# Performance work log

Hardware: AMD Instinct MI355X
Metric: run time of the kernel (lower is better)

## Reference

```python
import jax, jax.numpy as jnp
import numpy as np

ENC_DIM = 1024
NUM_HEADS = 16
HEAD_DIM = ENC_DIM // NUM_HEADS
D_FF = 4 * ENC_DIM
EPS = 1e-5


def _layernorm(x, g, b):
    mu = jnp.mean(x, axis=-1, keepdims=True)
    var = jnp.mean((x - mu) ** 2, axis=-1, keepdims=True)
    return (x - mu) * jax.lax.rsqrt(var + EPS) * g + b


def setup_inputs() -> dict:
    key = jax.random.key(0)
    ks = jax.random.split(key, 12)
    s = 1.0 / np.sqrt(ENC_DIM)
    sf = 1.0 / np.sqrt(D_FF)
    x = jax.random.normal(ks[0], (2, 2048, ENC_DIM), dtype=jnp.float32)
    return {
        "x": x,
        "ln1_g": jnp.ones((ENC_DIM,), jnp.float32),
        "ln1_b": jnp.zeros((ENC_DIM,), jnp.float32),
        "wq": jax.random.uniform(ks[1], (ENC_DIM, ENC_DIM), jnp.float32, -s, s),
        "bq": jax.random.uniform(ks[2], (ENC_DIM,), jnp.float32, -s, s),
        "wk": jax.random.uniform(ks[3], (ENC_DIM, ENC_DIM), jnp.float32, -s, s),
        "bk": jax.random.uniform(ks[4], (ENC_DIM,), jnp.float32, -s, s),
        "wv": jax.random.uniform(ks[5], (ENC_DIM, ENC_DIM), jnp.float32, -s, s),
        "bv": jax.random.uniform(ks[6], (ENC_DIM,), jnp.float32, -s, s),
        "wo": jax.random.uniform(ks[7], (ENC_DIM, ENC_DIM), jnp.float32, -s, s),
        "bo": jax.random.uniform(ks[8], (ENC_DIM,), jnp.float32, -s, s),
        "w1": jax.random.uniform(ks[9], (ENC_DIM, D_FF), jnp.float32, -s, s),
        "b1": jax.random.uniform(ks[10], (D_FF,), jnp.float32, -s, s),
        "w2": jax.random.uniform(ks[11], (D_FF, ENC_DIM), jnp.float32, -sf, sf),
        "b2": jnp.zeros((ENC_DIM,), jnp.float32),
        "ln2_g": jnp.ones((ENC_DIM,), jnp.float32),
        "ln2_b": jnp.zeros((ENC_DIM,), jnp.float32),
    }


def reference(x, ln1_g, ln1_b, wq, bq, wk, bk, wv, bv, wo, bo, w1, b1, w2, b2, ln2_g, ln2_b):
    B, S, D = x.shape
    h = _layernorm(x, ln1_g, ln1_b)
    # QKV projections -> (B, H, S, hd)
    def split_heads(t):
        return t.reshape(B, S, NUM_HEADS, HEAD_DIM).transpose(0, 2, 1, 3)
    q = split_heads(h @ wq + bq)
    k = split_heads(h @ wk + bk)
    v = split_heads(h @ wv + bv)
    scores = jnp.einsum("bhqd,bhkd->bhqk", q, k) / np.sqrt(HEAD_DIM)
    probs = jax.nn.softmax(scores, axis=-1)
    attn = jnp.einsum("bhqk,bhkd->bhqd", probs, v)
    attn = attn.transpose(0, 2, 1, 3).reshape(B, S, D)
    x = attn @ wo + bo + x  # residual 1
    h2 = _layernorm(x, ln2_g, ln2_b)
    mlp = jax.nn.gelu(h2 @ w1 + b1, approximate=False) @ w2 + b2
    return x + mlp
```

## Files before the change

kernel.cpp:

```cpp
#include <hip/hip_runtime.h>

typedef unsigned short u16;
typedef unsigned int u32;
typedef __bf16 bf16x8 __attribute__((ext_vector_type(8)));
typedef float floatx4 __attribute__((ext_vector_type(4)));

__device__ __forceinline__ u16 f2bf(float f) {
    u32 u = __float_as_uint(f);
    u = (u + 0x7FFFu + ((u >> 16) & 1u)) >> 16;
    return (u16)u;
}

__device__ __forceinline__ void gld_lds16(const u16* g, u16* l) {
    __builtin_amdgcn_global_load_lds(
        (const __attribute__((address_space(1))) u32*)g,
        (__attribute__((address_space(3))) u32*)l, 16, 0, 0);
}

__device__ __forceinline__ float gelu_exact(float v) {
    const float z = fabsf(v) * 0.70710678118f;
    const float t = __builtin_amdgcn_rcpf(1.0f + 0.3275911f * z);
    const float e = __builtin_amdgcn_exp2f(-z * z * 1.44269504f);
    float poly = 1.061405429f;
    poly = poly * t - 1.453152027f;
    poly = poly * t + 1.421413741f;
    poly = poly * t - 0.284496736f;
    poly = poly * t + 0.254829592f;
    float erfz = 1.0f - poly * t * e;
    erfz = copysignf(erfz, v);
    return 0.5f * v * (1.0f + erfz);
}

__global__ __launch_bounds__(256) void transpose_cvt4(
    const float* __restrict__ s0, const float* __restrict__ s1,
    const float* __restrict__ s2, const float* __restrict__ s3,
    u16* __restrict__ d0, u16* __restrict__ d1,
    u16* __restrict__ d2, u16* __restrict__ d3)
{
    __shared__ float t[32][33];
    const int z = blockIdx.z;
    const float* src = z == 0 ? s0 : (z == 1 ? s1 : (z == 2 ? s2 : s3));
    u16* dst = z == 0 ? d0 : (z == 1 ? d1 : (z == 2 ? d2 : d3));
    const int bm = blockIdx.x * 32, bk = blockIdx.y * 32;
    const int tx = threadIdx.x & 31, ty = threadIdx.x >> 5;
    #pragma unroll
    for (int i = ty; i < 32; i += 8)
        t[i][tx] = src[(long)(bk + i) * 1024 + bm + tx];
    __syncthreads();
    #pragma unroll
    for (int i = ty; i < 32; i += 8)
        dst[(long)(bm + i) * 1024 + bk + tx] = f2bf(t[tx][i]);
}

__global__ __launch_bounds__(256) void transpose_cvt(
    const float* __restrict__ src, u16* __restrict__ dst, int K, int M)
{
    __shared__ float t[32][33];
    const int bm = blockIdx.x * 32, bk = blockIdx.y * 32;
    const int tx = threadIdx.x & 31, ty = threadIdx.x >> 5;
    #pragma unroll
    for (int i = ty; i < 32; i += 8)
        t[i][tx] = src[(long)(bk + i) * M + bm + tx];
    __syncthreads();
    #pragma unroll
    for (int i = ty; i < 32; i += 8)
        dst[(long)(bm + i) * K + bk + tx] = f2bf(t[tx][i]);
}

__global__ __launch_bounds__(256) void ln_kernel(
    const float* __restrict__ x, const float* __restrict__ g,
    const float* __restrict__ bta, u16* __restrict__ out)
{
    const int row = blockIdx.x;
    const int tid = threadIdx.x;
    const float4 v = ((const float4*)(x + (long)row * 1024))[tid];
    float s  = v.x + v.y + v.z + v.w;
    float s2 = v.x*v.x + v.y*v.y + v.z*v.z + v.w*v.w;
    #pragma unroll
    for (int off = 1; off < 64; off <<= 1) {
        s  += __shfl_xor(s, off);
        s2 += __shfl_xor(s2, off);
    }
    __shared__ float red[8];
    const int wave = tid >> 6, lane = tid & 63;
    if (lane == 0) { red[wave] = s; red[4 + wave] = s2; }
    __syncthreads();
    s  = red[0] + red[1] + red[2] + red[3];
    s2 = red[4] + red[5] + red[6] + red[7];
    const float mu   = s * (1.0f / 1024.0f);
    const float var  = s2 * (1.0f / 1024.0f) - mu * mu;
    const float rstd = rsqrtf(var + 1e-5f);
    const int c = tid << 2;
    ushort4 o;
    o.x = f2bf((v.x - mu) * rstd * g[c + 0] + bta[c + 0]);
    o.y = f2bf((v.y - mu) * rstd * g[c + 1] + bta[c + 1]);
    o.z = f2bf((v.z - mu) * rstd * g[c + 2] + bta[c + 2]);
    o.w = f2bf((v.w - mu) * rstd * g[c + 3] + bta[c + 3]);
    ((ushort4*)(out + (long)row * 1024))[tid] = o;
}

__global__ __launch_bounds__(256) void add_kernel(
    float* __restrict__ out, const float* __restrict__ p1)
{
    const int t = blockIdx.x * 256 + threadIdx.x;
    const float4 a = ((const float4*)out)[t];
    const float4 c = ((const float4*)p1)[t];
    float4 o;
    o.x = a.x + c.x;
    o.y = a.y + c.y;
    o.z = a.z + c.z;
    o.w = a.w + c.w;
    ((float4*)out)[t] = o;
}

__global__ __launch_bounds__(256) void vtrans_kernel(
    const u16* __restrict__ V, u16* __restrict__ Vt)
{
    __shared__ u16 t[64][72];
    const int bh = blockIdx.y, s0 = blockIdx.x << 6;
    const int tid = threadIdx.x;
    const long base = (long)bh * 2048 * 64;
    const int row = tid >> 2, seg = tid & 3;
    *(uint4*)&t[row][seg << 3] =
        *(const uint4*)(V + base + (long)(s0 + row) * 64 + (seg << 3));
    *(uint4*)&t[row][(seg + 4) << 3] =
        *(const uint4*)(V + base + (long)(s0 + row) * 64 + ((seg + 4) << 3));
    __syncthreads();
    #pragma unroll
    for (int half = 0; half < 2; ++half) {
        const int sl = (seg + (half << 2)) << 3;
        u16 tmp[8];
        #pragma unroll
        for (int j = 0; j < 8; ++j) tmp[j] = t[sl + j][row];
        *(uint4*)(Vt + base + (long)row * 2048 + s0 + sl) = *(uint4*)tmp;
    }
}

template<int MODE, int BN>
__global__ __launch_bounds__(256) void gemm_kernel(
    const u16* __restrict__ A, const u16* __restrict__ Bt,
    const float* __restrict__ bias0, const float* __restrict__ bias1,
    const float* __restrict__ bias2, const float* __restrict__ res,
    float* __restrict__ part1, void* __restrict__ outv, int K, int M)
{
    constexpr int MS  = (BN == 128) ? 4 : 2;
    constexpr int NIB = (BN == 128) ? 4 : 2;
    constexpr int DB  = (BN == 128) ? 2 : 1;
    __shared__ u16 As[DB][128 * 64];
    __shared__ u16 Bs[DB][BN * 64];
    const int tid = threadIdx.x, lane = tid & 63, wave = tid >> 6;
    const int wm = (BN == 128) ? ((wave >> 1) << 6) : (wave << 5);
    const int wn = (BN == 128) ? ((wave & 1) << 6) : 0;
    const int lrow = lane & 15, quad = lane >> 4;
    const int sl = lrow & 7;

    const int nwg = gridDim.x * gridDim.y * gridDim.z;
    const int lin = blockIdx.x + gridDim.x * (blockIdx.y + gridDim.y * blockIdx.z);
    const int wg  = (lin & 7) * (nwg >> 3) + (lin >> 3);
    const int bx  = wg % gridDim.x;
    const int rest = wg / gridDim.x;
    const int by  = rest % gridDim.y;
    const int bz  = rest / gridDim.y;

    const long rowbase = (long)by * 128;
    const long colbase = (long)bx * BN;
    int kstart = 0, kend = K;
    if constexpr (MODE == 3) {
        kstart = bz * (K >> 1);
        kend   = kstart + (K >> 1);
    }

    const u16* gA[4]; int lA[4];
    #pragma unroll
    for (int i = 0; i < 4; ++i) {
        const int cid = (i << 6) + lane;
        const int rl = cid >> 3, p = cid & 7, q = p ^ (rl & 7);
        gA[i] = A + (rowbase + (wave << 5) + rl) * (long)K + kstart + (q << 3);
        lA[i] = ((wave << 5) + rl) * 64 + (p << 3);
    }
    const u16* gB[NIB]; int lB[NIB];
    #pragma unroll
    for (int i = 0; i < NIB; ++i) {
        const int cid = (i << 6) + lane;
        const int rl = cid >> 3, p = cid & 7, q = p ^ (rl & 7);
        const int rw = (BN == 128) ? (wave << 5) : (wave << 4);
        gB[i] = Bt + (colbase + rw + rl) * (long)K + kstart + (q << 3);
        lB[i] = (rw + rl) * 64 + (p << 3);
    }

    floatx4 acc[MS][4];
    #pragma unroll
    for (int i = 0; i < MS; ++i)
        #pragma unroll
        for (int j = 0; j < 4; ++j)
            acc[i][j] = floatx4{0.f, 0.f, 0.f, 0.f};

    if constexpr (DB == 2) {
        #pragma unroll
        for (int i = 0; i < 4; ++i) { gld_lds16(gA[i], As[0] + lA[i]); gA[i] += 64; }
        #pragma unroll
        for (int i = 0; i < NIB; ++i) { gld_lds16(gB[i], Bs[0] + lB[i]); gB[i] += 64; }

        const int niter = (kend - kstart) >> 6;
        int cur = 0;
        for (int t = 0; t < niter; ++t) {
            if (t + 1 < niter) {
                #pragma unroll
                for (int i = 0; i < 4; ++i) { gld_lds16(gA[i], As[cur ^ 1] + lA[i]); gA[i] += 64; }
                #pragma unroll
                for (int i = 0; i < NIB; ++i) { gld_lds16(gB[i], Bs[cur ^ 1] + lB[i]); gB[i] += 64; }
                asm volatile("s_waitcnt vmcnt(8)" ::: "memory");
            } else {
                asm volatile("s_waitcnt vmcnt(0)" ::: "memory");
            }
            __builtin_amdgcn_s_barrier();

            const u16* as = As[cur];
            const u16* bs = Bs[cur];
            #pragma unroll
            for (int kc = 0; kc < 2; ++kc) {
                const int ph = (((kc << 2) + quad) ^ sl) << 3;
                bf16x8 af[MS], bf[4];
                #pragma unroll
                for (int ms = 0; ms < MS; ++ms)
                    af[ms] = *(const bf16x8*)&as[(wm + (ms << 4) + lrow) * 64 + ph];
                #pragma unroll
                for (int ns = 0; ns < 4; ++ns)
                    bf[ns] = *(const bf16x8*)&bs[(wn + (ns << 4) + lrow) * 64 + ph];
                #pragma unroll
                for (int ms = 0; ms < MS; ++ms)
                    #pragma unroll
                    for (int ns = 0; ns < 4; ++ns)
                        acc[ms][ns] = __builtin_amdgcn_mfma_f32_16x16x32_bf16(
                            af[ms], bf[ns], acc[ms][ns], 0, 0, 0);
            }
            asm volatile("s_waitcnt lgkmcnt(0)" ::: "memory");
            __builtin_amdgcn_s_barrier();
            cur ^= 1;
        }
    } else {
        for (int k0 = kstart; k0 < kend; k0 += 64) {
            __syncthreads();
            #pragma unroll
            for (int i = 0; i < 4; ++i) { gld_lds16(gA[i], As[0] + lA[i]); gA[i] += 64; }
            #pragma unroll
            for (int i = 0; i < NIB; ++i) { gld_lds16(gB[i], Bs[0] + lB[i]); gB[i] += 64; }
            __syncthreads();
            #pragma unroll
            for (int kc = 0; kc < 2; ++kc) {
                const int ph = (((kc << 2) + quad) ^ sl) << 3;
                bf16x8 af[MS], bf[4];
                #pragma unroll
                for (int ms = 0; ms < MS; ++ms)
                    af[ms] = *(const bf16x8*)&As[0][(wm + (ms << 4) + lrow) * 64 + ph];
                #pragma unroll
                for (int ns = 0; ns < 4; ++ns)
                    bf[ns] = *(const bf16x8*)&Bs[0][(wn + (ns << 4) + lrow) * 64 + ph];
                #pragma unroll
                for (int ms = 0; ms < MS; ++ms)
                    #pragma unroll
                    for (int ns = 0; ns < 4; ++ns)
                        acc[ms][ns] = __builtin_amdgcn_mfma_f32_16x16x32_bf16(
                            af[ms], bf[ns], acc[ms][ns], 0, 0, 0);
            }
        }
    }

    float* tgt = nullptr;
    if constexpr (MODE == 3) tgt = bz ? part1 : (float*)outv;
    #pragma unroll
    for (int ms = 0; ms < MS; ++ms) {
        #pragma unroll
        for (int ns = 0; ns < 4; ++ns) {
            const long col = colbase + wn + (ns << 4) + lrow;
            float bv = 0.f;
            if constexpr (MODE == 0) {
                const int which = (int)(col >> 10);
                const float* bp = which == 0 ? bias0 : (which == 1 ? bias1 : bias2);
                bv = bp[col & 1023];
            } else if constexpr (MODE == 1 || MODE == 2) {
                bv = bias0[col];
            }
            #pragma unroll
            for (int r = 0; r < 4; ++r) {
                const long row = rowbase + wm + (ms << 4) + (quad << 2) + r;
                float v = acc[ms][ns][r] + bv;
                if constexpr (MODE == 0) {
                    const long which = col >> 10;
                    if (which == 0) v *= 0.18033688f;
                    const long b = row >> 11, s = row & 2047;
                    const long h = (col >> 6) & 15, d = col & 63;
                    ((u16*)outv)[which * 4194304 + (((b << 4) + h) * 2048 + s) * 64 + d] = f2bf(v);
                } else if constexpr (MODE == 1) {
                    const long idx = row * M + col;
                    ((float*)outv)[idx] = v + res[idx];
                } else if constexpr (MODE == 2) {
                    ((u16*)outv)[row * M + col] = f2bf(gelu_exact(v));
                } else {
                    const long idx = row * M + col;
                    if (bz == 0)
                        tgt[idx] = v + bias0[col] + res[idx];
                    else
                        tgt[idx] = v;
                }
            }
        }
    }
}

__global__ __launch_bounds__(512) void attn_kernel(
    const u16* __restrict__ Q, const u16* __restrict__ Kp,
    const u16* __restrict__ Vt, u16* __restrict__ O)
{
    __shared__ u16 Ks[2][4096];
    __shared__ u16 Vs[2][4096];
    __shared__ u16 Ps[8][16][72];
    const int tid = threadIdx.x, lane = tid & 63, wave = tid >> 6;
    const int lrow = lane & 15, quad = lane >> 4;

    const int lin = blockIdx.x;
    const int nl  = ((lin & 7) << 6) + (lin >> 3);
    const int bh  = nl >> 4;
    const int qt  = nl & 15;
    const long kvbase = (long)bh * 2048 * 64;
    const int qbase = (qt << 7) + (wave << 4);

    const int srow = lane >> 3;
    const int schunk = (lane & 7) ^ srow;
    const int c = wave & 3;
    const bool isV = wave >= 4;
    const int lofs = c << 10;
    const u16* g0 = isV
        ? (Vt + kvbase + (long)(((c << 4) + srow) * 2048 + (schunk << 3)))
        : (Kp + kvbase + (long)(((c << 4) + srow) * 64   + (schunk << 3)));
    const u16* g1 = g0 + (isV ? 8 * 2048 : 8 * 64);
    const int gstep = isV ? 64 : 4096;
    u16* lb0 = isV ? &Vs[0][lofs] : &Ks[0][lofs];
    u16* lb1 = isV ? &Vs[1][lofs] : &Ks[1][lofs];

    bf16x8 qf[2];
    #pragma unroll
    for (int h = 0; h < 2; ++h)
        qf[h] = *(const bf16x8*)(Q + kvbase +
            (long)(qbase + lrow) * 64 + (quad << 3) + (h << 5));

    int aoff[4][2];
    #pragma unroll
    for (int ns = 0; ns < 4; ++ns)
        #pragma unroll
        for (int h = 0; h < 2; ++h)
            aoff[ns][h] = ((ns << 4) + lrow) * 64 +
                          (((quad + (h << 2)) ^ (lrow & 7)) << 3);

    floatx4 oacc[4];
    #pragma unroll
    for (int ns = 0; ns < 4; ++ns)
        oacc[ns] = floatx4{0.f, 0.f, 0.f, 0.f};
    float lr = 0.f;

    gld_lds16(g0, lb0);
    gld_lds16(g1, lb0 + 512);
    g0 += gstep; g1 += gstep;

    for (int it = 0; it < 32; ++it) {
        const int cur = it & 1;
        __syncthreads();
        if (it < 31) {
            u16* dst = cur ? lb0 : lb1;
            gld_lds16(g0, dst);
            gld_lds16(g1, dst + 512);
            g0 += gstep; g1 += gstep;
        }
        const u16* ks = &Ks[cur][0];
        const u16* vs = &Vs[cur][0];

        floatx4 st[4];
        __builtin_amdgcn_s_setprio(1);
        #pragma unroll
        for (int ns = 0; ns < 4; ++ns) {
            const bf16x8 af0 = *(const bf16x8*)&ks[aoff[ns][0]];
            const bf16x8 af1 = *(const bf16x8*)&ks[aoff[ns][1]];
            floatx4 z = floatx4{0.f, 0.f, 0.f, 0.f};
            st[ns] = __builtin_amdgcn_mfma_f32_16x16x32_bf16(af0, qf[0], z, 0, 0, 0);
            st[ns] = __builtin_amdgcn_mfma_f32_16x16x32_bf16(af1, qf[1], st[ns], 0, 0, 0);
        }
        __builtin_amdgcn_s_setprio(0);

        float rs = 0.f;
        #pragma unroll
        for (int ns = 0; ns < 4; ++ns) {
            const float p0 = __builtin_amdgcn_exp2f(st[ns][0]);
            const float p1 = __builtin_amdgcn_exp2f(st[ns][1]);
            const float p2 = __builtin_amdgcn_exp2f(st[ns][2]);
            const float p3 = __builtin_amdgcn_exp2f(st[ns][3]);
            rs += (p0 + p1) + (p2 + p3);
            uint2 w;
            w.x = __builtin_amdgcn_perm(__float_as_uint(p1) + 0x8000u,
                                        __float_as_uint(p0) + 0x8000u, 0x07060302u);
            w.y = __builtin_amdgcn_perm(__float_as_uint(p3) + 0x8000u,
                                        __float_as_uint(p2) + 0x8000u, 0x07060302u);
            *(uint2*)&Ps[wave][lrow][(ns << 4) + (quad << 2)] = w;
        }
        rs += __shfl_xor(rs, 16);
        rs += __shfl_xor(rs, 32);
        lr += rs;
        const bf16x8 pf0 = *(const bf16x8*)&Ps[wave][lrow][quad << 3];
        const bf16x8 pf1 = *(const bf16x8*)&Ps[wave][lrow][(quad << 3) + 32];

        __builtin_amdgcn_s_setprio(1);
        #pragma unroll
        for (int ns = 0; ns < 4; ++ns) {
            const bf16x8 vf0 = *(const bf16x8*)&vs[aoff[ns][0]];
            const bf16x8 vf1 = *(const bf16x8*)&vs[aoff[ns][1]];
            oacc[ns] = __builtin_amdgcn_mfma_f32_16x16x32_bf16(pf0, vf0, oacc[ns], 0, 0, 0);
            oacc[ns] = __builtin_amdgcn_mfma_f32_16x16x32_bf16(pf1, vf1, oacc[ns], 0, 0, 0);
        }
        __builtin_amdgcn_s_setprio(0);
    }

    const int b = bh >> 4, h = bh & 15;
    float linv[4];
    #pragma unroll
    for (int r = 0; r < 4; ++r)
        linv[r] = 1.0f / __shfl(lr, (quad << 2) + r);
    #pragma unroll
    for (int ns = 0; ns < 4; ++ns)
        #pragma unroll
        for (int r = 0; r < 4; ++r) {
            const int q = qbase + (quad << 2) + r;
            const long token = (long)b * 2048 + q;
            O[token * 1024 + (h << 6) + (ns << 4) + lrow] =
                f2bf(oacc[ns][r] * linv[r]);
        }
}

extern "C" void kernel_launch(void* const* d_in, const int* in_sizes, int n_in,
                              void* d_out, int out_size, void* d_ws, size_t ws_size,
                              hipStream_t stream)
{
    const float* x     = (const float*)d_in[0];
    const float* ln1_g = (const float*)d_in[1];
    const float* ln1_b = (const float*)d_in[2];
    const float* wq    = (const float*)d_in[3];
    const float* bq    = (const float*)d_in[4];
    const float* wk    = (const float*)d_in[5];
    const float* bk    = (const float*)d_in[6];
    const float* wv    = (const float*)d_in[7];
    const float* bv    = (const float*)d_in[8];
    const float* wo    = (const float*)d_in[9];
    const float* bo    = (const float*)d_in[10];
    const float* w1    = (const float*)d_in[11];
    const float* b1    = (const float*)d_in[12];
    const float* w2    = (const float*)d_in[13];
    const float* b2    = (const float*)d_in[14];
    const float* ln2_g = (const float*)d_in[15];
    const float* ln2_b = (const float*)d_in[16];
    float* out = (float*)d_out;

    char* w = (char*)d_ws;
    const size_t MB = 1024 * 1024;
    u16*   wqkvt = (u16*)(w + 0);
    u16*   wot   = (u16*)(w + 6  * MB);
    u16*   w1t   = (u16*)(w + 8  * MB);
    u16*   w2t   = (u16*)(w + 16 * MB);
    u16*   h1    = (u16*)(w + 24 * MB);
    u16*   qkvb  = (u16*)(w + 32 * MB);
    u16*   vtb   = (u16*)(w + 56 * MB);
    float* x1    = (float*)(w + 64 * MB);
    float* part1 = (float*)(w + 80 * MB);
    u16*   ffb   = (u16*)(w + 32 * MB);
    u16*   qb = qkvb;
    u16*   kb = qkvb + 4194304;
    u16*   vb = qkvb + 8388608;

    transpose_cvt4<<<dim3(32, 32, 4), 256, 0, stream>>>(
        wq, wk, wv, wo, wqkvt, wqkvt + 1048576, wqkvt + 2097152, wot);
    transpose_cvt<<<dim3(128, 32), 256, 0, stream>>>(w1, w1t, 1024, 4096);
    transpose_cvt<<<dim3(32, 128), 256, 0, stream>>>(w2, w2t, 4096, 1024);

    ln_kernel<<<4096, 256, 0, stream>>>(x, ln1_g, ln1_b, h1);

    gemm_kernel<0, 128><<<dim3(24, 32), 256, 0, stream>>>(
        h1, wqkvt, bq, bk, bv, nullptr, nullptr, qkvb, 1024, 3072);

    vtrans_kernel<<<dim3(32, 32), 256, 0, stream>>>(vb, vtb);

    attn_kernel<<<dim3(512), 512, 0, stream>>>(qb, kb, vtb, h1);

    gemm_kernel<1, 64><<<dim3(16, 32), 256, 0, stream>>>(
        h1, wot, bo, nullptr, nullptr, x, nullptr, x1, 1024, 1024);

    ln_kernel<<<4096, 256, 0, stream>>>(x1, ln2_g, ln2_b, h1);

    gemm_kernel<2, 128><<<dim3(32, 32), 256, 0, stream>>>(
        h1, w1t, b1, nullptr, nullptr, nullptr, nullptr, ffb, 1024, 4096);

    gemm_kernel<3, 128><<<dim3(8, 32, 2), 256, 0, stream>>>(
        ffb, w2t, b2, nullptr, nullptr, x1, part1, out, 4096, 1024);

    add_kernel<<<4096, 256, 0, stream>>>(out, part1);
}
```

Baseline: 372.9 us.

## Use 256x256 tiled GEMM with 8 waves and atomic split-K for FFN down

Replaces the 128-row GEMM kernel with a 512-thread 256x256 tile kernel (double-buffered LDS, setprio around MFMA bursts) for QKV, FFN-up and FFN-down, which raises data reuse per tile. FFN-down now uses 4-way split-K accumulated via float atomicAdd into a memset output, replacing the separate partial buffer and add kernel. The O-projection keeps the old 64-wide tile path as a standalone kernel. Larger tiles reduce the number of workgroups and may hurt occupancy, and float atomics make the summation order nondeterministic.

```diff
diff --git a/kernel.cpp b/kernel.cpp
--- a/kernel.cpp
+++ b/kernel.cpp
@@ -99,20 +99,6 @@
     ((ushort4*)(out + (long)row * 1024))[tid] = o;
 }
 
-__global__ __launch_bounds__(256) void add_kernel(
-    float* __restrict__ out, const float* __restrict__ p1)
-{
-    const int t = blockIdx.x * 256 + threadIdx.x;
-    const float4 a = ((const float4*)out)[t];
-    const float4 c = ((const float4*)p1)[t];
-    float4 o;
-    o.x = a.x + c.x;
-    o.y = a.y + c.y;
-    o.z = a.z + c.z;
-    o.w = a.w + c.w;
-    ((float4*)out)[t] = o;
-}
-
 __global__ __launch_bounds__(256) void vtrans_kernel(
     const u16* __restrict__ V, u16* __restrict__ Vt)
 {
@@ -136,23 +122,18 @@
     }
 }
 
-template<int MODE, int BN>
-__global__ __launch_bounds__(256) void gemm_kernel(
+template<int MODE>
+__global__ __launch_bounds__(512, 2) void gemm256_kernel(
     const u16* __restrict__ A, const u16* __restrict__ Bt,
     const float* __restrict__ bias0, const float* __restrict__ bias1,
     const float* __restrict__ bias2, const float* __restrict__ res,
-    float* __restrict__ part1, void* __restrict__ outv, int K, int M)
-{
-    constexpr int MS  = (BN == 128) ? 4 : 2;
-    constexpr int NIB = (BN == 128) ? 4 : 2;
-    constexpr int DB  = (BN == 128) ? 2 : 1;
-    __shared__ u16 As[DB][128 * 64];
-    __shared__ u16 Bs[DB][BN * 64];
+    float* __restrict__ outf, void* __restrict__ outv, int K, int M)
+{
+    __shared__ u16 As[2][256 * 64];
+    __shared__ u16 Bs[2][256 * 64];
     const int tid = threadIdx.x, lane = tid & 63, wave = tid >> 6;
-    const int wm = (BN == 128) ? ((wave >> 1) << 6) : (wave << 5);
-    const int wn = (BN == 128) ? ((wave & 1) << 6) : 0;
-    const int lrow = lane & 15, quad = lane >> 4;
-    const int sl = lrow & 7;
+    const int wr = wave >> 2, wc = wave & 3;
+    const int lrow = lane & 15, quad = lane >> 4, sl = lrow & 7;
 
     const int nwg = gridDim.x * gridDim.y * gridDim.z;
     const int lin = blockIdx.x + gridDim.x * (blockIdx.y + gridDim.y * blockIdx.z);
@@ -162,128 +143,103 @@
     const int by  = rest % gridDim.y;
     const int bz  = rest / gridDim.y;
 
-    const long rowbase = (long)by * 128;
-    const long colbase = (long)bx * BN;
+    const long rowbase = (long)by * 256;
+    const long colbase = (long)bx * 256;
     int kstart = 0, kend = K;
-    if constexpr (MODE == 3) {
-        kstart = bz * (K >> 1);
-        kend   = kstart + (K >> 1);
-    }
+    if constexpr (MODE == 3) { kstart = bz * (K >> 2); kend = kstart + (K >> 2); }
 
     const u16* gA[4]; int lA[4];
+    const u16* gB[4]; int lB[4];
     #pragma unroll
     for (int i = 0; i < 4; ++i) {
-        const int cid = (i << 6) + lane;
+        const int cid = (i << 9) + tid;
         const int rl = cid >> 3, p = cid & 7, q = p ^ (rl & 7);
-        gA[i] = A + (rowbase + (wave << 5) + rl) * (long)K + kstart + (q << 3);
-        lA[i] = ((wave << 5) + rl) * 64 + (p << 3);
-    }
-    const u16* gB[NIB]; int lB[NIB];
-    #pragma unroll
-    for (int i = 0; i < NIB; ++i) {
-        const int cid = (i << 6) + lane;
-        const int rl = cid >> 3, p = cid & 7, q = p ^ (rl & 7);
-        const int rw = (BN == 128) ? (wave << 5) : (wave << 4);
-        gB[i] = Bt + (colbase + rw + rl) * (long)K + kstart + (q << 3);
-        lB[i] = (rw + rl) * 64 + (p << 3);
-    }
-
-    floatx4 acc[MS][4];
-    #pragma unroll
-    for (int i = 0; i < MS; ++i)
+        gA[i] = A  + (rowbase + rl) * (long)K + kstart + (q << 3);
+        gB[i] = Bt + (colbase + rl) * (long)K + kstart + (q << 3);
+        lA[i] = rl * 64 + (p << 3);
+        lB[i] = rl * 64 + (p << 3);
+    }
+
+    floatx4 acc[8][4];
+    #pragma unroll
+    for (int i = 0; i < 8; ++i)
         #pragma unroll
         for (int j = 0; j < 4; ++j)
             acc[i][j] = floatx4{0.f, 0.f, 0.f, 0.f};
 
-    if constexpr (DB == 2) {
-        #pragma unroll
-        for (int i = 0; i < 4; ++i) { gld_lds16(gA[i], As[0] + lA[i]); gA[i] += 64; }
-        #pragma unroll
-        for (int i = 0; i < NIB; ++i) { gld_lds16(gB[i], Bs[0] + lB[i]); gB[i] += 64; }
-
-        const int niter = (kend - kstart) >> 6;
-        int cur = 0;
-        for (int t = 0; t < niter; ++t) {
-            if (t + 1 < niter) {
+    #pragma unroll
+    for (int i = 0; i < 4; ++i) { gld_lds16(gA[i], As[0] + lA[i]); gA[i] += 64; }
+    #pragma unroll
+    for (int i = 0; i < 4; ++i) { gld_lds16(gB[i], Bs[0] + lB[i]); gB[i] += 64; }
+    asm volatile("s_waitcnt vmcnt(0)" ::: "memory");
+    __builtin_amdgcn_s_barrier();
+    __builtin_amdgcn_sched_barrier(0);
+
+    const int niter = (kend - kstart) >> 6;
+    int cur = 0;
+    for (int t = 0; t < niter; ++t) {
+        if (t + 1 < niter) {
+            #pragma unroll
+            for (int i = 0; i < 4; ++i) { gld_lds16(gA[i], As[cur ^ 1] + lA[i]); gA[i] += 64; }
+            #pragma unroll
+            for (int i = 0; i < 4; ++i) { gld_lds16(gB[i], Bs[cur ^ 1] + lB[i]); gB[i] += 64; }
+        }
+
+        const u16* as = As[cur];
+        const u16* bs = Bs[cur];
+
+        bf16x8 bfr[4][2];
+        #pragma unroll
+        for (int ns = 0; ns < 4; ++ns)
+            #pragma unroll
+            for (int kc = 0; kc < 2; ++kc)
+                bfr[ns][kc] = *(const bf16x8*)
+                    &bs[((wc << 6) + (ns << 4) + lrow) * 64 + ((((kc << 2) + quad) ^ sl) << 3)];
+
+        #pragma unroll
+        for (int p = 0; p < 4; ++p) {
+            bf16x8 af[2][2];
+            #pragma unroll
+            for (int m = 0; m < 2; ++m)
                 #pragma unroll
-                for (int i = 0; i < 4; ++i) { gld_lds16(gA[i], As[cur ^ 1] + lA[i]); gA[i] += 64; }
+                for (int kc = 0; kc < 2; ++kc)
+                    af[m][kc] = *(const bf16x8*)
+                        &as[((wr << 7) + ((p * 2 + m) << 4) + lrow) * 64 + ((((kc << 2) + quad) ^ sl) << 3)];
+            __builtin_amdgcn_s_setprio(1);
+            #pragma unroll
+            for (int kc = 0; kc < 2; ++kc)
                 #pragma unroll
-                for (int i = 0; i < NIB; ++i) { gld_lds16(gB[i], Bs[cur ^ 1] + lB[i]); gB[i] += 64; }
-                asm volatile("s_waitcnt vmcnt(8)" ::: "memory");
-            } else {
-                asm volatile("s_waitcnt vmcnt(0)" ::: "memory");
-            }
-            __builtin_amdgcn_s_barrier();
-
-            const u16* as = As[cur];
-            const u16* bs = Bs[cur];
-            #pragma unroll
-            for (int kc = 0; kc < 2; ++kc) {
-                const int ph = (((kc << 2) + quad) ^ sl) << 3;
-                bf16x8 af[MS], bf[4];
-                #pragma unroll
-                for (int ms = 0; ms < MS; ++ms)
-                    af[ms] = *(const bf16x8*)&as[(wm + (ms << 4) + lrow) * 64 + ph];
-                #pragma unroll
-                for (int ns = 0; ns < 4; ++ns)
-                    bf[ns] = *(const bf16x8*)&bs[(wn + (ns << 4) + lrow) * 64 + ph];
-                #pragma unroll
-                for (int ms = 0; ms < MS; ++ms)
+                for (int m = 0; m < 2; ++m)
                     #pragma unroll
                     for (int ns = 0; ns < 4; ++ns)
-                        acc[ms][ns] = __builtin_amdgcn_mfma_f32_16x16x32_bf16(
-                            af[ms], bf[ns], acc[ms][ns], 0, 0, 0);
-            }
-            asm volatile("s_waitcnt lgkmcnt(0)" ::: "memory");
-            __builtin_amdgcn_s_barrier();
-            cur ^= 1;
-        }
-    } else {
-        for (int k0 = kstart; k0 < kend; k0 += 64) {
-            __syncthreads();
-            #pragma unroll
-            for (int i = 0; i < 4; ++i) { gld_lds16(gA[i], As[0] + lA[i]); gA[i] += 64; }
-            #pragma unroll
-            for (int i = 0; i < NIB; ++i) { gld_lds16(gB[i], Bs[0] + lB[i]); gB[i] += 64; }
-            __syncthreads();
-            #pragma unroll
-            for (int kc = 0; kc < 2; ++kc) {
-                const int ph = (((kc << 2) + quad) ^ sl) << 3;
-                bf16x8 af[MS], bf[4];
-                #pragma unroll
-                for (int ms = 0; ms < MS; ++ms)
-                    af[ms] = *(const bf16x8*)&As[0][(wm + (ms << 4) + lrow) * 64 + ph];
-                #pragma unroll
-                for (int ns = 0; ns < 4; ++ns)
-                    bf[ns] = *(const bf16x8*)&Bs[0][(wn + (ns << 4) + lrow) * 64 + ph];
-                #pragma unroll
-                for (int ms = 0; ms < MS; ++ms)
-                    #pragma unroll
-                    for (int ns = 0; ns < 4; ++ns)
-                        acc[ms][ns] = __builtin_amdgcn_mfma_f32_16x16x32_bf16(
-                            af[ms], bf[ns], acc[ms][ns], 0, 0, 0);
-            }
-        }
-    }
-
-    float* tgt = nullptr;
-    if constexpr (MODE == 3) tgt = bz ? part1 : (float*)outv;
-    #pragma unroll
-    for (int ms = 0; ms < MS; ++ms) {
+                        acc[p * 2 + m][ns] = __builtin_amdgcn_mfma_f32_16x16x32_bf16(
+                            af[m][kc], bfr[ns][kc], acc[p * 2 + m][ns], 0, 0, 0);
+            __builtin_amdgcn_s_setprio(0);
+        }
+
+        asm volatile("s_waitcnt lgkmcnt(0)" ::: "memory");
+        asm volatile("s_waitcnt vmcnt(0)" ::: "memory");
+        __builtin_amdgcn_s_barrier();
+        __builtin_amdgcn_sched_barrier(0);
+        cur ^= 1;
+    }
+
+    #pragma unroll
+    for (int ms = 0; ms < 8; ++ms) {
         #pragma unroll
         for (int ns = 0; ns < 4; ++ns) {
-            const long col = colbase + wn + (ns << 4) + lrow;
+            const long col = colbase + (wc << 6) + (ns << 4) + lrow;
             float bv = 0.f;
             if constexpr (MODE == 0) {
                 const int which = (int)(col >> 10);
                 const float* bp = which == 0 ? bias0 : (which == 1 ? bias1 : bias2);
                 bv = bp[col & 1023];
-            } else if constexpr (MODE == 1 || MODE == 2) {
+            } else if constexpr (MODE == 2) {
                 bv = bias0[col];
             }
             #pragma unroll
             for (int r = 0; r < 4; ++r) {
-                const long row = rowbase + wm + (ms << 4) + (quad << 2) + r;
+                const long row = rowbase + (wr << 7) + (ms << 4) + (quad << 2) + r;
                 float v = acc[ms][ns][r] + bv;
                 if constexpr (MODE == 0) {
                     const long which = col >> 10;
@@ -291,18 +247,101 @@
                     const long b = row >> 11, s = row & 2047;
                     const long h = (col >> 6) & 15, d = col & 63;
                     ((u16*)outv)[which * 4194304 + (((b << 4) + h) * 2048 + s) * 64 + d] = f2bf(v);
-                } else if constexpr (MODE == 1) {
-                    const long idx = row * M + col;
-                    ((float*)outv)[idx] = v + res[idx];
                 } else if constexpr (MODE == 2) {
                     ((u16*)outv)[row * M + col] = f2bf(gelu_exact(v));
                 } else {
                     const long idx = row * M + col;
-                    if (bz == 0)
-                        tgt[idx] = v + bias0[col] + res[idx];
-                    else
-                        tgt[idx] = v;
+                    if (bz == 0) v += bias0[col] + res[idx];
+                    atomicAdd(&outf[idx], v);
                 }
+            }
+        }
+    }
+}
+
+__global__ __launch_bounds__(256) void gemm_oproj_kernel(
+    const u16* __restrict__ A, const u16* __restrict__ Bt,
+    const float* __restrict__ bias0, const float* __restrict__ res,
+    float* __restrict__ out, int K, int M)
+{
+    constexpr int MS = 2, NIB = 2;
+    __shared__ u16 As[128 * 64];
+    __shared__ u16 Bs[64 * 64];
+    const int tid = threadIdx.x, lane = tid & 63, wave = tid >> 6;
+    const int wm = wave << 5, wn = 0;
+    const int lrow = lane & 15, quad = lane >> 4;
+    const int sl = lrow & 7;
+
+    const int nwg = gridDim.x * gridDim.y;
+    const int lin = blockIdx.x + gridDim.x * blockIdx.y;
+    const int wg  = (lin & 7) * (nwg >> 3) + (lin >> 3);
+    const int bx  = wg % gridDim.x;
+    const int by  = wg / gridDim.x;
+
+    const long rowbase = (long)by * 128;
+    const long colbase = (long)bx * 64;
+
+    const u16* gA[4]; int lA[4];
+    #pragma unroll
+    for (int i = 0; i < 4; ++i) {
+        const int cid = (i << 6) + lane;
+        const int rl = cid >> 3, p = cid & 7, q = p ^ (rl & 7);
+        gA[i] = A + (rowbase + (wave << 5) + rl) * (long)K + (q << 3);
+        lA[i] = ((wave << 5) + rl) * 64 + (p << 3);
+    }
+    const u16* gB[NIB]; int lB[NIB];
+    #pragma unroll
+    for (int i = 0; i < NIB; ++i) {
+        const int cid = (i << 6) + lane;
+        const int rl = cid >> 3, p = cid & 7, q = p ^ (rl & 7);
+        gB[i] = Bt + (colbase + (wave << 4) + rl) * (long)K + (q << 3);
+        lB[i] = ((wave << 4) + rl) * 64 + (p << 3);
+    }
+
+    floatx4 acc[MS][4];
+    #pragma unroll
+    for (int i = 0; i < MS; ++i)
+        #pragma unroll
+        for (int j = 0; j < 4; ++j)
+            acc[i][j] = floatx4{0.f, 0.f, 0.f, 0.f};
+
+    for (int k0 = 0; k0 < K; k0 += 64) {
+        __syncthreads();
+        #pragma unroll
+        for (int i = 0; i < 4; ++i) { gld_lds16(gA[i], As + lA[i]); gA[i] += 64; }
+        #pragma unroll
+        for (int i = 0; i < NIB; ++i) { gld_lds16(gB[i], Bs + lB[i]); gB[i] += 64; }
+        __syncthreads();
+        #pragma unroll
+        for (int kc = 0; kc < 2; ++kc) {
+            const int ph = (((kc << 2) + quad) ^ sl) << 3;
+            bf16x8 af[MS], bf[4];
+            #pragma unroll
+            for (int ms = 0; ms < MS; ++ms)
+                af[ms] = *(const bf16x8*)&As[(wm + (ms << 4) + lrow) * 64 + ph];
+            #pragma unroll
+            for (int ns = 0; ns < 4; ++ns)
+                bf[ns] = *(const bf16x8*)&Bs[(wn + (ns << 4) + lrow) * 64 + ph];
+            #pragma unroll
+            for (int ms = 0; ms < MS; ++ms)
+                #pragma unroll
+                for (int ns = 0; ns < 4; ++ns)
+                    acc[ms][ns] = __builtin_amdgcn_mfma_f32_16x16x32_bf16(
+                        af[ms], bf[ns], acc[ms][ns], 0, 0, 0);
+        }
+    }
+
+    #pragma unroll
+    for (int ms = 0; ms < MS; ++ms) {
+        #pragma unroll
+        for (int ns = 0; ns < 4; ++ns) {
+            const long col = colbase + wn + (ns << 4) + lrow;
+            const float bv = bias0[col];
+            #pragma unroll
+            for (int r = 0; r < 4; ++r) {
+                const long row = rowbase + wm + (ms << 4) + (quad << 2) + r;
+                const long idx = row * M + col;
+                out[idx] = acc[ms][ns][r] + bv + res[idx];
             }
         }
     }
@@ -467,7 +506,6 @@
     u16*   qkvb  = (u16*)(w + 32 * MB);
     u16*   vtb   = (u16*)(w + 56 * MB);
     float* x1    = (float*)(w + 64 * MB);
-    float* part1 = (float*)(w + 80 * MB);
     u16*   ffb   = (u16*)(w + 32 * MB);
     u16*   qb = qkvb;
     u16*   kb = qkvb + 4194304;
@@ -480,23 +518,22 @@
 
     ln_kernel<<<4096, 256, 0, stream>>>(x, ln1_g, ln1_b, h1);
 
-    gemm_kernel<0, 128><<<dim3(24, 32), 256, 0, stream>>>(
+    gemm256_kernel<0><<<dim3(12, 16), 512, 0, stream>>>(
         h1, wqkvt, bq, bk, bv, nullptr, nullptr, qkvb, 1024, 3072);
 
     vtrans_kernel<<<dim3(32, 32), 256, 0, stream>>>(vb, vtb);
 
     attn_kernel<<<dim3(512), 512, 0, stream>>>(qb, kb, vtb, h1);
 
-    gemm_kernel<1, 64><<<dim3(16, 32), 256, 0, stream>>>(
-        h1, wot, bo, nullptr, nullptr, x, nullptr, x1, 1024, 1024);
+    gemm_oproj_kernel<<<dim3(16, 32), 256, 0, stream>>>(
+        h1, wot, bo, x, x1, 1024, 1024);
 
     ln_kernel<<<4096, 256, 0, stream>>>(x1, ln2_g, ln2_b, h1);
 
-    gemm_kernel<2, 128><<<dim3(32, 32), 256, 0, stream>>>(
+    gemm256_kernel<2><<<dim3(16, 16), 512, 0, stream>>>(
         h1, w1t, b1, nullptr, nullptr, nullptr, nullptr, ffb, 1024, 4096);
 
-    gemm_kernel<3, 128><<<dim3(8, 32, 2), 256, 0, stream>>>(
-        ffb, w2t, b2, nullptr, nullptr, x1, part1, out, 4096, 1024);
-
-    add_kernel<<<4096, 256, 0, stream>>>(out, part1);
-}
+    hipMemsetAsync(out, 0, (size_t)4096 * 1024 * 4, stream);
+    gemm256_kernel<3><<<dim3(4, 16, 4), 512, 0, stream>>>(
+        ffb, w2t, b2, nullptr, nullptr, x1, out, nullptr, 4096, 1024);
+}
```

After: 407.4 us. +9.2%, slower.

## Add 256x256-tile 8-wave GEMM kernel for QKV and FFN1 projections

Applied to the files above, without the earlier changes.

Adds a new GEMM kernel with 256x256 output tiles, 512 threads and double-buffered LDS (global-to-LDS direct loads with an XOR swizzle). It replaces the 128x128-tile kernel for the QKV projection and the first FFN layer, and removes those modes from the old kernel. The larger tiles raise arithmetic intensity and cut redundant global loads of A and B. The cost is far fewer workgroups (192 for QKV, 256 for FFN1), which can leave CUs idle or unbalanced, plus roughly 128KB of LDS per block, which limits occupancy.

```diff
diff --git a/kernel.cpp b/kernel.cpp
--- a/kernel.cpp
+++ b/kernel.cpp
@@ -136,11 +136,138 @@
     }
 }
 
+template<int MODE>
+__global__ __launch_bounds__(512, 2) void gemm256_kernel(
+    const u16* __restrict__ A, const u16* __restrict__ Bt,
+    const float* __restrict__ bias0, const float* __restrict__ bias1,
+    const float* __restrict__ bias2, void* __restrict__ outv, int K, int M)
+{
+    __shared__ u16 As[2][256 * 64];
+    __shared__ u16 Bs[2][256 * 64];
+    const int tid = threadIdx.x, lane = tid & 63, wave = tid >> 6;
+    const int wr = wave >> 2, wc = wave & 3;
+    const int lrow = lane & 15, quad = lane >> 4, sl = lrow & 7;
+
+    const int nwg = gridDim.x * gridDim.y;
+    const int lin = blockIdx.x + gridDim.x * blockIdx.y;
+    const int wg  = (lin & 7) * (nwg >> 3) + (lin >> 3);
+    const int bx  = wg % gridDim.x;
+    const int by  = wg / gridDim.x;
+
+    const long rowbase = (long)by * 256;
+    const long colbase = (long)bx * 256;
+
+    const u16* gA[4]; int lA[4];
+    const u16* gB[4]; int lB[4];
+    #pragma unroll
+    for (int i = 0; i < 4; ++i) {
+        const int cid = (i << 9) + tid;
+        const int rl = cid >> 3, p = cid & 7, q = p ^ (rl & 7);
+        gA[i] = A  + (rowbase + rl) * (long)K + (q << 3);
+        gB[i] = Bt + (colbase + rl) * (long)K + (q << 3);
+        lA[i] = rl * 64 + (p << 3);
+        lB[i] = rl * 64 + (p << 3);
+    }
+
+    floatx4 acc[8][4];
+    #pragma unroll
+    for (int i = 0; i < 8; ++i)
+        #pragma unroll
+        for (int j = 0; j < 4; ++j)
+            acc[i][j] = floatx4{0.f, 0.f, 0.f, 0.f};
+
+    #pragma unroll
+    for (int i = 0; i < 4; ++i) { gld_lds16(gA[i], As[0] + lA[i]); gA[i] += 64; }
+    #pragma unroll
+    for (int i = 0; i < 4; ++i) { gld_lds16(gB[i], Bs[0] + lB[i]); gB[i] += 64; }
+    asm volatile("s_waitcnt vmcnt(0)" ::: "memory");
+    __builtin_amdgcn_s_barrier();
+    __builtin_amdgcn_sched_barrier(0);
+
+    const int niter = K >> 6;
+    int cur = 0;
+    for (int t = 0; t < niter; ++t) {
+        if (t + 1 < niter) {
+            #pragma unroll
+            for (int i = 0; i < 4; ++i) { gld_lds16(gA[i], As[cur ^ 1] + lA[i]); gA[i] += 64; }
+            #pragma unroll
+            for (int i = 0; i < 4; ++i) { gld_lds16(gB[i], Bs[cur ^ 1] + lB[i]); gB[i] += 64; }
+        }
+
+        const u16* as = As[cur];
+        const u16* bs = Bs[cur];
+
+        bf16x8 bfr[4][2];
+        #pragma unroll
+        for (int ns = 0; ns < 4; ++ns)
+            #pragma unroll
+            for (int kc = 0; kc < 2; ++kc)
+                bfr[ns][kc] = *(const bf16x8*)
+                    &bs[((wc << 6) + (ns << 4) + lrow) * 64 + ((((kc << 2) + quad) ^ sl) << 3)];
+
+        #pragma unroll
+        for (int p = 0; p < 4; ++p) {
+            bf16x8 af[2][2];
+            #pragma unroll
+            for (int m = 0; m < 2; ++m)
+                #pragma unroll
+                for (int kc = 0; kc < 2; ++kc)
+                    af[m][kc] = *(const bf16x8*)
+                        &as[((wr << 7) + ((p * 2 + m) << 4) + lrow) * 64 + ((((kc << 2) + quad) ^ sl) << 3)];
+            __builtin_amdgcn_s_setprio(1);
+            #pragma unroll
+            for (int kc = 0; kc < 2; ++kc)
+                #pragma unroll
+                for (int m = 0; m < 2; ++m)
+                    #pragma unroll
+                    for (int ns = 0; ns < 4; ++ns)
+                        acc[p * 2 + m][ns] = __builtin_amdgcn_mfma_f32_16x16x32_bf16(
+                            af[m][kc], bfr[ns][kc], acc[p * 2 + m][ns], 0, 0, 0);
+            __builtin_amdgcn_s_setprio(0);
+        }
+
+        asm volatile("s_waitcnt lgkmcnt(0)" ::: "memory");
+        asm volatile("s_waitcnt vmcnt(0)" ::: "memory");
+        __builtin_amdgcn_s_barrier();
+        __builtin_amdgcn_sched_barrier(0);
+        cur ^= 1;
+    }
+
+    #pragma unroll
+    for (int ms = 0; ms < 8; ++ms) {
+        #pragma unroll
+        for (int ns = 0; ns < 4; ++ns) {
+            const long col = colbase + (wc << 6) + (ns << 4) + lrow;
+            float bv;
+            if constexpr (MODE == 0) {
+                const int which = (int)(col >> 10);
+                const float* bp = which == 0 ? bias0 : (which == 1 ? bias1 : bias2);
+                bv = bp[col & 1023];
+            } else {
+                bv = bias0[col];
+            }
+            #pragma unroll
+            for (int r = 0; r < 4; ++r) {
+                const long row = rowbase + (wr << 7) + (ms << 4) + (quad << 2) + r;
+                float v = acc[ms][ns][r] + bv;
+                if constexpr (MODE == 0) {
+                    const long which = col >> 10;
+                    if (which == 0) v *= 0.18033688f;
+                    const long b = row >> 11, s = row & 2047;
+                    const long h = (col >> 6) & 15, d = col & 63;
+                    ((u16*)outv)[which * 4194304 + (((b << 4) + h) * 2048 + s) * 64 + d] = f2bf(v);
+                } else {
+                    ((u16*)outv)[row * M + col] = f2bf(gelu_exact(v));
+                }
+            }
+        }
+    }
+}
+
 template<int MODE, int BN>
 __global__ __launch_bounds__(256) void gemm_kernel(
     const u16* __restrict__ A, const u16* __restrict__ Bt,
-    const float* __restrict__ bias0, const float* __restrict__ bias1,
-    const float* __restrict__ bias2, const float* __restrict__ res,
+    const float* __restrict__ bias0, const float* __restrict__ res,
     float* __restrict__ part1, void* __restrict__ outv, int K, int M)
 {
     constexpr int MS  = (BN == 128) ? 4 : 2;
@@ -274,28 +401,14 @@
         for (int ns = 0; ns < 4; ++ns) {
             const long col = colbase + wn + (ns << 4) + lrow;
             float bv = 0.f;
-            if constexpr (MODE == 0) {
-                const int which = (int)(col >> 10);
-                const float* bp = which == 0 ? bias0 : (which == 1 ? bias1 : bias2);
-                bv = bp[col & 1023];
-            } else if constexpr (MODE == 1 || MODE == 2) {
-                bv = bias0[col];
-            }
+            if constexpr (MODE == 1) bv = bias0[col];
             #pragma unroll
             for (int r = 0; r < 4; ++r) {
                 const long row = rowbase + wm + (ms << 4) + (quad << 2) + r;
                 float v = acc[ms][ns][r] + bv;
-                if constexpr (MODE == 0) {
-                    const long which = col >> 10;
-                    if (which == 0) v *= 0.18033688f;
-                    const long b = row >> 11, s = row & 2047;
-                    const long h = (col >> 6) & 15, d = col & 63;
-                    ((u16*)outv)[which * 4194304 + (((b << 4) + h) * 2048 + s) * 64 + d] = f2bf(v);
-                } else if constexpr (MODE == 1) {
+                if constexpr (MODE == 1) {
                     const long idx = row * M + col;
                     ((float*)outv)[idx] = v + res[idx];
-                } else if constexpr (MODE == 2) {
-                    ((u16*)outv)[row * M + col] = f2bf(gelu_exact(v));
                 } else {
                     const long idx = row * M + col;
                     if (bz == 0)
@@ -480,23 +593,23 @@
 
     ln_kernel<<<4096, 256, 0, stream>>>(x, ln1_g, ln1_b, h1);
 
-    gemm_kernel<0, 128><<<dim3(24, 32), 256, 0, stream>>>(
-        h1, wqkvt, bq, bk, bv, nullptr, nullptr, qkvb, 1024, 3072);
+    gemm256_kernel<0><<<dim3(12, 16), 512, 0, stream>>>(
+        h1, wqkvt, bq, bk, bv, qkvb, 1024, 3072);
 
     vtrans_kernel<<<dim3(32, 32), 256, 0, stream>>>(vb, vtb);
 
     attn_kernel<<<dim3(512), 512, 0, stream>>>(qb, kb, vtb, h1);
 
     gemm_kernel<1, 64><<<dim3(16, 32), 256, 0, stream>>>(
-        h1, wot, bo, nullptr, nullptr, x, nullptr, x1, 1024, 1024);
+        h1, wot, bo, x, nullptr, x1, 1024, 1024);
 
     ln_kernel<<<4096, 256, 0, stream>>>(x1, ln2_g, ln2_b, h1);
 
-    gemm_kernel<2, 128><<<dim3(32, 32), 256, 0, stream>>>(
-        h1, w1t, b1, nullptr, nullptr, nullptr, nullptr, ffb, 1024, 4096);
+    gemm256_kernel<2><<<dim3(16, 16), 512, 0, stream>>>(
+        h1, w1t, b1, nullptr, nullptr, ffb, 1024, 4096);
 
     gemm_kernel<3, 128><<<dim3(8, 32, 2), 256, 0, stream>>>(
-        ffb, w2t, b2, nullptr, nullptr, x1, part1, out, 4096, 1024);
+        ffb, w2t, b2, x1, part1, out, 4096, 1024);
 
     add_kernel<<<4096, 256, 0, stream>>>(out, part1);
 }
```

Measured after the change: 363.0 us. 1.03x faster.
